# Performance work log

Hardware: AMD Instinct MI355X
Metric: run time of the kernel (lower is better)

## Reference

```python
import jax, jax.numpy as jnp
import numpy as np

B, S, D_IN, D_OUT = 4, 2048, 1024, 1024


def setup_inputs() -> dict:
    key = jax.random.key(0)
    ks = jax.random.split(key, 6)
    scale = 1.0 / np.sqrt(D_IN)
    return {
        "inputs_for_keys": jax.random.normal(ks[0], (B, S, D_IN), jnp.float32),
        "inputs_for_values": jax.random.normal(ks[1], (B, S, D_IN), jnp.float32),
        "inputs_for_queries": jax.random.normal(ks[2], (B, S, D_IN), jnp.float32),
        "WK": jax.random.uniform(ks[3], (D_IN, D_OUT), jnp.float32, -scale, scale),
        "WQ": jax.random.uniform(ks[4], (D_IN, D_OUT), jnp.float32, -scale, scale),
        "WV": jax.random.uniform(ks[5], (D_IN, D_OUT), jnp.float32, -scale, scale),
    }


def reference(inputs_for_keys, inputs_for_values, inputs_for_queries, WK, WQ, WV):
    # QKV projections: [B,S,Din] @ [Din,Dout] -> [B,S,Dout]
    keys = jnp.einsum("bsd,de->bse", inputs_for_keys, WK)
    values = jnp.einsum("bsd,de->bse", inputs_for_values, WV)
    queries = jnp.einsum("bsd,de->bse", inputs_for_queries, WQ)
    d_k = keys.shape[-1]
    # scaled scores [B,S,S]
    scores = jnp.einsum("bqe,bke->bqk", queries, keys) / jnp.sqrt(jnp.float32(d_k))
    # causal mask: position k > q gets -inf (strictly upper triangular)
    q_idx = jnp.arange(S)[:, None]
    k_idx = jnp.arange(S)[None, :]
    scores = jnp.where(k_idx > q_idx, -jnp.inf, scores)
    att = jax.nn.softmax(scores, axis=-1)
    out = jnp.einsum("bqk,bke->bqe", att, values)  # [B,S,Dout]
    return out
```

## Files before the change

kernel.cpp:

```cpp
#include <hip/hip_runtime.h>
#include <stdint.h>


typedef __attribute__((ext_vector_type(8))) short short8;
typedef __attribute__((ext_vector_type(8))) unsigned short ushort8;
typedef __attribute__((ext_vector_type(4))) float f32x4;

__device__ __forceinline__ unsigned short f2bf(float f) {
  union { float f; unsigned u; } v; v.f = f;
  unsigned u = v.u + 0x7FFFu + ((v.u >> 16) & 1u);
  return (unsigned short)(u >> 16);
}
__device__ __forceinline__ float bf2f(unsigned short h) {
  union { unsigned u; float f; } v; v.u = ((unsigned)h) << 16;
  return v.f;
}

__device__ __forceinline__ void gload16(const void* g, void* l) {
  __builtin_amdgcn_global_load_lds(
      (const __attribute__((address_space(1))) unsigned int*)g,
      (__attribute__((address_space(3))) unsigned int*)l, 16, 0, 0);
}

template<int N> __device__ __forceinline__ void vmwait() {
  static_assert(N >= 0 && N <= 8, "vmcnt range");
  if constexpr (N == 0) asm volatile("s_waitcnt vmcnt(0)" ::: "memory");
  else if constexpr (N == 1) asm volatile("s_waitcnt vmcnt(1)" ::: "memory");
  else if constexpr (N == 2) asm volatile("s_waitcnt vmcnt(2)" ::: "memory");
  else if constexpr (N == 3) asm volatile("s_waitcnt vmcnt(3)" ::: "memory");
  else if constexpr (N == 4) asm volatile("s_waitcnt vmcnt(4)" ::: "memory");
  else if constexpr (N == 5) asm volatile("s_waitcnt vmcnt(5)" ::: "memory");
  else if constexpr (N == 6) asm volatile("s_waitcnt vmcnt(6)" ::: "memory");
  else if constexpr (N == 7) asm volatile("s_waitcnt vmcnt(7)" ::: "memory");
  else asm volatile("s_waitcnt vmcnt(8)" ::: "memory");
}
__device__ __forceinline__ void barrier_() { asm volatile("s_barrier" ::: "memory"); }
__device__ __forceinline__ void lgkm0() { asm volatile("s_waitcnt lgkmcnt(0)" ::: "memory"); }

__global__ __launch_bounds__(256)
void cvt3_bf16(const float* __restrict__ Xq, const float* __restrict__ Xk,
               const float* __restrict__ Xv,
               unsigned short* __restrict__ Oq, unsigned short* __restrict__ Ok,
               unsigned short* __restrict__ Ov) {
  const int bx = blockIdx.x;
  const int op = bx >> 12, r = bx & 4095;
  const float* in = op == 0 ? Xq : op == 1 ? Xk : Xv;
  unsigned short* out = op == 0 ? Oq : op == 1 ? Ok : Ov;
  const long i = ((long)r * 256 + threadIdx.x) * 8;
  float4 a = *(const float4*)(in + i);
  float4 b = *(const float4*)(in + i + 4);
  ushort8 rr;
  rr[0] = f2bf(a.x); rr[1] = f2bf(a.y); rr[2] = f2bf(a.z); rr[3] = f2bf(a.w);
  rr[4] = f2bf(b.x); rr[5] = f2bf(b.y); rr[6] = f2bf(b.z); rr[7] = f2bf(b.w);
  *(ushort8*)(out + i) = rr;
}

__global__ __launch_bounds__(256)
void wtrans3(const float* __restrict__ WQ, const float* __restrict__ WK,
             const float* __restrict__ WV,
             unsigned short* __restrict__ WQT, unsigned short* __restrict__ WKT,
             unsigned short* __restrict__ WVT) {
  const int z = blockIdx.z;
  const float* W = z == 0 ? WQ : z == 1 ? WK : WV;
  unsigned short* WT = z == 0 ? WQT : z == 1 ? WKT : WVT;
  const float scale = z == 0 ? 0.03125f : 1.0f;
  __shared__ float t[32][33];
  const int bk = blockIdx.x * 32, be = blockIdx.y * 32;
  const int tx = threadIdx.x, ty = threadIdx.y;
#pragma unroll
  for (int j = 0; j < 32; j += 8)
    t[ty + j][tx] = W[(long)(bk + ty + j) * 1024 + (be + tx)];
  __syncthreads();
#pragma unroll
  for (int j = 0; j < 32; j += 8)
    WT[(long)(be + ty + j) * 1024 + (bk + tx)] = f2bf(t[tx][ty + j] * scale);
}

template<typename CT, int MF, int NF>
__device__ __forceinline__ void gemm_body(const unsigned short* __restrict__ A,
                                          const unsigned short* __restrict__ B,
                                          CT* __restrict__ C,
                                          int bm, int bn, int kmax,
                                          int lda, int ldb, int ldc,
                                          char* AL, char* BL) {
  constexpr int BM = MF * 32, BN = NF * 64;
  constexpr int LA = BM / 128, LB = BN / 128;
  constexpr int V = 2 * LA + LB;

  const int tid = threadIdx.x;
  const int lane = tid & 63, wid = tid >> 6;
  const int wr = wid >> 2, wc = wid & 3;
  const int fr = lane & 15, fq = lane >> 4;
  const int srow = tid >> 2;
  const int scol = (((tid & 3) ^ ((tid >> 3) & 3)) << 3);
  const int m0 = bm * BM, n0 = bn * BN;
  const int nt = kmax >> 6;

  f32x4 acc[MF][NF] = {};

  const unsigned short* As = A + (long)(m0 + srow) * lda + scol;
  const unsigned short* Bs = B + (long)(n0 + srow) * ldb + scol;

  auto stageA = [&](int b, int h, int kt) {
#pragma unroll
    for (int l = 0; l < LA; ++l)
      gload16(As + (long)l * 128 * lda + kt * 64 + h * 32,
              AL + b * (BM * 128) + h * (BM * 64) + l * 8192 + tid * 16);
  };
  auto stageB = [&](int b, int h, int kt) {
#pragma unroll
    for (int l = 0; l < LB; ++l)
      gload16(Bs + (long)l * 128 * ldb + kt * 64 + h * 32,
              BL + b * (BN * 128) + h * (BN * 64) + l * 8192 + tid * 16);
  };

  const int aoff = (wr * (BM / 2) + fr) * 64 + ((fq ^ ((fr >> 1) & 3)) << 4);
  const int boff = (wc * (BN / 4) + fr) * 64 + ((fq ^ ((fr >> 1) & 3)) << 4);
  auto ardf = [&](int b, int kk, int m) -> short8 {
    return *(const short8*)(AL + b * (BM * 128) + kk * (BM * 64) + aoff + m * 1024);
  };
  auto brdf = [&](int b, int kk, int n) -> short8 {
    return *(const short8*)(BL + b * (BN * 128) + kk * (BN * 64) + boff + n * 1024);
  };

  stageA(0, 0, 0); stageB(0, 0, 0); stageA(0, 1, 0); stageB(0, 1, 0);

  for (int u = 0; u < nt; ++u) {
    const int cb = u & 1, nb = cb ^ 1;
    const bool pf = (u + 1 < nt);
    lgkm0();
    barrier_();
    if (pf) { stageA(nb, 0, u + 1); vmwait<V>(); }
    else    { vmwait<LA + LB>(); }
    barrier_();
    short8 bfr[NF], af[MF / 2];
#pragma unroll
    for (int n = 0; n < NF; ++n) bfr[n] = brdf(cb, 0, n);
#pragma unroll
    for (int m = 0; m < MF / 2; ++m) af[m] = ardf(cb, 0, m);
    if (pf) stageB(nb, 0, u + 1);
    __builtin_amdgcn_s_setprio(1);
#pragma unroll
    for (int m = 0; m < MF / 2; ++m)
#pragma unroll
      for (int n = 0; n < NF; ++n)
        acc[m][n] = __builtin_amdgcn_mfma_f32_16x16x32_bf16(af[m], bfr[n], acc[m][n], 0, 0, 0);
    __builtin_amdgcn_s_setprio(0);
#pragma unroll
    for (int m = 0; m < MF / 2; ++m) af[m] = ardf(cb, 0, MF / 2 + m);
    if (pf) stageA(nb, 1, u + 1);
    __builtin_amdgcn_s_setprio(1);
#pragma unroll
    for (int m = 0; m < MF / 2; ++m)
#pragma unroll
      for (int n = 0; n < NF; ++n)
        acc[MF / 2 + m][n] =
            __builtin_amdgcn_mfma_f32_16x16x32_bf16(af[m], bfr[n], acc[MF / 2 + m][n], 0, 0, 0);
    __builtin_amdgcn_s_setprio(0);
    if (pf) vmwait<V>(); else vmwait<0>();
    barrier_();
#pragma unroll
    for (int n = 0; n < NF; ++n) bfr[n] = brdf(cb, 1, n);
#pragma unroll
    for (int m = 0; m < MF / 2; ++m) af[m] = ardf(cb, 1, m);
    if (pf) stageB(nb, 1, u + 1);
    __builtin_amdgcn_s_setprio(1);
#pragma unroll
    for (int m = 0; m < MF / 2; ++m)
#pragma unroll
      for (int n = 0; n < NF; ++n)
        acc[m][n] = __builtin_amdgcn_mfma_f32_16x16x32_bf16(af[m], bfr[n], acc[m][n], 0, 0, 0);
    __builtin_amdgcn_s_setprio(0);
#pragma unroll
    for (int m = 0; m < MF / 2; ++m) af[m] = ardf(cb, 1, MF / 2 + m);
    __builtin_amdgcn_s_setprio(1);
#pragma unroll
    for (int m = 0; m < MF / 2; ++m)
#pragma unroll
      for (int n = 0; n < NF; ++n)
        acc[MF / 2 + m][n] =
            __builtin_amdgcn_mfma_f32_16x16x32_bf16(af[m], bfr[n], acc[MF / 2 + m][n], 0, 0, 0);
    __builtin_amdgcn_s_setprio(0);
  }

#pragma unroll
  for (int m = 0; m < MF; ++m) {
    const int row = m0 + wr * (BM / 2) + m * 16 + fq * 4;
#pragma unroll
    for (int n = 0; n < NF; ++n) {
      const int col = n0 + wc * (BN / 4) + n * 16 + fr;
#pragma unroll
      for (int r = 0; r < 4; ++r) {
        float v = acc[m][n][r];
        if constexpr (sizeof(CT) == 2)
          C[(long)(row + r) * ldc + col] = (CT)f2bf(v);
        else
          C[(long)(row + r) * ldc + col] = (CT)v;
      }
    }
  }
}

__global__ __launch_bounds__(512, 2)
void qkvt_gemm(const unsigned short* __restrict__ Xq, const unsigned short* __restrict__ WQT,
               unsigned short* __restrict__ Q,
               const unsigned short* __restrict__ Xk, const unsigned short* __restrict__ WKT,
               unsigned short* __restrict__ Kk,
               const unsigned short* __restrict__ WVT, const unsigned short* __restrict__ Xv,
               unsigned short* __restrict__ VT) {
  __shared__ __align__(16) char pool[131072];
  const int id = (blockIdx.x & 7) * 32 + (blockIdx.x >> 3);
  if (id < 128)
    gemm_body<unsigned short, 8, 4>(Xq, WQT, Q, id >> 2, id & 3, 1024,
                                    1024, 1024, 1024, pool, pool + 65536);
  else
    gemm_body<unsigned short, 8, 4>(Xk, WKT, Kk, (id - 128) >> 2, id & 3, 1024,
                                    1024, 1024, 1024, pool, pool + 65536);
  __syncthreads();
  gemm_body<unsigned short, 4, 4>(WVT, Xv, VT, id >> 5, id & 31, 1024,
                                  1024, 1024, 8192, pool, pool + 32768);
}

__global__ __launch_bounds__(512, 2)
void scores_gemm(const unsigned short* __restrict__ Q, const unsigned short* __restrict__ K,
                 unsigned short* __restrict__ S) {
  __shared__ __align__(16) char pool[131072];
  const int id = (blockIdx.x & 7) * 32 + (blockIdx.x >> 3);
  const int bz = id >> 6, r = id & 63, bm = r >> 3, bn = r & 7;
  if (bn > bm) return;
  gemm_body<unsigned short, 8, 4>(Q + (long)bz * 2048 * 1024, K + (long)bz * 2048 * 1024,
                                  S + (long)bz * 2048 * 2048, bm, bn, 1024,
                                  1024, 1024, 2048, pool, pool + 65536);
}

__global__ __launch_bounds__(512, 4)
void pv_gemm(const unsigned short* __restrict__ P, const unsigned short* __restrict__ VT,
             float* __restrict__ O) {
  __shared__ __align__(16) char pool[65536];
  const int b = blockIdx.x;
  int bm, r;
  if (b < 256) { bm = 15 - (b >> 5); r = b & 31; }
  else         { bm = (b - 256) >> 5; r = b & 31; }
  const int bn = r & 7, bz = r >> 3;
  gemm_body<float, 4, 2>(P + (long)bz * 2048 * 2048, VT + (long)bz * 2048,
                         O + (long)bz * 2048 * 1024, bm, bn, (bm + 1) * 128,
                         2048, 8192, 1024, pool, pool + 32768);
}

__global__ __launch_bounds__(256)
void softmax_causal(unsigned short* __restrict__ P) {
  const int row = blockIdx.x;
  const int q = row & 2047;
  unsigned short* p = P + (long)row * 2048;
  const int nfill = ((q >> 7) + 1) << 7;
  const int tid = threadIdx.x;
  const int lane = tid & 63, wid = tid >> 6;
  const int i0 = tid * 8;
  __shared__ float red[8];

  float v[8];
  float lmax = -3.0e38f;
  if (i0 <= q) {
    ushort8 v8 = *(const ushort8*)(p + i0);
#pragma unroll
    for (int j = 0; j < 8; ++j) {
      float f = bf2f(v8[j]);
      f = (i0 + j <= q) ? f : -3.0e38f;
      v[j] = f;
      lmax = fmaxf(lmax, f);
    }
  } else {
#pragma unroll
    for (int j = 0; j < 8; ++j) v[j] = -3.0e38f;
  }
#pragma unroll
  for (int off = 1; off < 64; off <<= 1)
    lmax = fmaxf(lmax, __shfl_xor(lmax, off));
  if (lane == 0) red[wid] = lmax;
  __syncthreads();
  const float mx = fmaxf(fmaxf(red[0], red[1]), fmaxf(red[2], red[3]));

  float lsum = 0.f;
#pragma unroll
  for (int j = 0; j < 8; ++j) {
    float e = __expf(v[j] - mx);
    v[j] = e;
    lsum += e;
  }
#pragma unroll
  for (int off = 1; off < 64; off <<= 1)
    lsum += __shfl_xor(lsum, off);
  if (lane == 0) red[4 + wid] = lsum;
  __syncthreads();
  const float inv = 1.0f / (red[4] + red[5] + red[6] + red[7]);

  if (i0 < nfill) {
    ushort8 r;
#pragma unroll
    for (int j = 0; j < 8; ++j)
      r[j] = (i0 + j <= q) ? f2bf(v[j] * inv) : (unsigned short)0;
    *(ushort8*)(p + i0) = r;
  }
}

extern "C" void kernel_launch(void* const* d_in, const int* in_sizes, int n_in,
                              void* d_out, int out_size, void* d_ws, size_t ws_size,
                              hipStream_t stream) {
  const float* Xk = (const float*)d_in[0];
  const float* Xv = (const float*)d_in[1];
  const float* Xq = (const float*)d_in[2];
  const float* WK = (const float*)d_in[3];
  const float* WQ = (const float*)d_in[4];
  const float* WV = (const float*)d_in[5];
  float* out = (float*)d_out;

  unsigned short* ws = (unsigned short*)d_ws;
  const long NE = 8L * 1024 * 1024;
  unsigned short* Xqb = ws + 0 * NE;
  unsigned short* Xkb = ws + 1 * NE;
  unsigned short* Xvb = ws + 2 * NE;
  unsigned short* Qb  = ws + 3 * NE;
  unsigned short* Kb  = ws + 4 * NE;
  unsigned short* VTb = ws + 5 * NE;
  unsigned short* WQT = ws + 6 * NE;
  unsigned short* WKT = WQT + 1024 * 1024;
  unsigned short* WVT = WKT + 1024 * 1024;
  unsigned short* Sc  = ws;

  dim3 b256(256), b512(512);
  cvt3_bf16<<<12288, b256, 0, stream>>>(Xq, Xk, Xv, Xqb, Xkb, Xvb);
  wtrans3<<<dim3(32, 32, 3), dim3(32, 8), 0, stream>>>(WQ, WK, WV, WQT, WKT, WVT);
  qkvt_gemm<<<256, b512, 0, stream>>>(Xqb, WQT, Qb, Xkb, WKT, Kb, WVT, Xvb, VTb);
  scores_gemm<<<256, b512, 0, stream>>>(Qb, Kb, Sc);
  softmax_causal<<<8192, b256, 0, stream>>>(Sc);
  pv_gemm<<<512, b512, 0, stream>>>(Sc, VTb, out);
}
```

Baseline: 157.2 us.

## Restructure GEMM main loop to whole-tile prefetch and shrink scores tiles

```diff
diff --git a/kernel.cpp b/kernel.cpp
--- a/kernel.cpp
+++ b/kernel.cpp
@@ -23,7 +23,7 @@
 }
 
 template<int N> __device__ __forceinline__ void vmwait() {
-  static_assert(N >= 0 && N <= 8, "vmcnt range");
+  static_assert(N >= 0 && N <= 16, "vmcnt range");
   if constexpr (N == 0) asm volatile("s_waitcnt vmcnt(0)" ::: "memory");
   else if constexpr (N == 1) asm volatile("s_waitcnt vmcnt(1)" ::: "memory");
   else if constexpr (N == 2) asm volatile("s_waitcnt vmcnt(2)" ::: "memory");
@@ -32,7 +32,10 @@
   else if constexpr (N == 5) asm volatile("s_waitcnt vmcnt(5)" ::: "memory");
   else if constexpr (N == 6) asm volatile("s_waitcnt vmcnt(6)" ::: "memory");
   else if constexpr (N == 7) asm volatile("s_waitcnt vmcnt(7)" ::: "memory");
-  else asm volatile("s_waitcnt vmcnt(8)" ::: "memory");
+  else if constexpr (N == 8) asm volatile("s_waitcnt vmcnt(8)" ::: "memory");
+  else if constexpr (N == 10) asm volatile("s_waitcnt vmcnt(10)" ::: "memory");
+  else if constexpr (N == 12) asm volatile("s_waitcnt vmcnt(12)" ::: "memory");
+  else asm volatile("s_waitcnt vmcnt(16)" ::: "memory");
 }
 __device__ __forceinline__ void barrier_() { asm volatile("s_barrier" ::: "memory"); }
 __device__ __forceinline__ void lgkm0() { asm volatile("s_waitcnt lgkmcnt(0)" ::: "memory"); }
@@ -85,7 +88,9 @@
                                           char* AL, char* BL) {
   constexpr int BM = MF * 32, BN = NF * 64;
   constexpr int LA = BM / 128, LB = BN / 128;
-  constexpr int V = 2 * LA + LB;
+  constexpr int SA = 2 * (LA + LB);
+  constexpr int NH = (NF >= 4) ? 2 : 1;
+  constexpr int NS = NF / NH;
 
   const int tid = threadIdx.x;
   const int lane = tid & 63, wid = tid >> 6;
@@ -101,17 +106,18 @@
   const unsigned short* As = A + (long)(m0 + srow) * lda + scol;
   const unsigned short* Bs = B + (long)(n0 + srow) * ldb + scol;
 
-  auto stageA = [&](int b, int h, int kt) {
-#pragma unroll
-    for (int l = 0; l < LA; ++l)
-      gload16(As + (long)l * 128 * lda + kt * 64 + h * 32,
-              AL + b * (BM * 128) + h * (BM * 64) + l * 8192 + tid * 16);
-  };
-  auto stageB = [&](int b, int h, int kt) {
-#pragma unroll
-    for (int l = 0; l < LB; ++l)
-      gload16(Bs + (long)l * 128 * ldb + kt * 64 + h * 32,
-              BL + b * (BN * 128) + h * (BN * 64) + l * 8192 + tid * 16);
+  auto stageTile = [&](int b, int kt) {
+#pragma unroll
+    for (int h = 0; h < 2; ++h) {
+#pragma unroll
+      for (int l = 0; l < LA; ++l)
+        gload16(As + (long)l * 128 * lda + kt * 64 + h * 32,
+                AL + b * (BM * 128) + h * (BM * 64) + l * 8192 + tid * 16);
+#pragma unroll
+      for (int l = 0; l < LB; ++l)
+        gload16(Bs + (long)l * 128 * ldb + kt * 64 + h * 32,
+                BL + b * (BN * 128) + h * (BN * 64) + l * 8192 + tid * 16);
+    }
   };
 
   const int aoff = (wr * (BM / 2) + fr) * 64 + ((fq ^ ((fr >> 1) & 3)) << 4);
@@ -123,64 +129,44 @@
     return *(const short8*)(BL + b * (BN * 128) + kk * (BN * 64) + boff + n * 1024);
   };
 
-  stageA(0, 0, 0); stageB(0, 0, 0); stageA(0, 1, 0); stageB(0, 1, 0);
+  stageTile(0, 0);
 
   for (int u = 0; u < nt; ++u) {
     const int cb = u & 1, nb = cb ^ 1;
-    const bool pf = (u + 1 < nt);
     lgkm0();
     barrier_();
-    if (pf) { stageA(nb, 0, u + 1); vmwait<V>(); }
-    else    { vmwait<LA + LB>(); }
+    if (u + 1 < nt) { stageTile(nb, u + 1); vmwait<SA>(); }
+    else            { vmwait<0>(); }
     barrier_();
-    short8 bfr[NF], af[MF / 2];
-#pragma unroll
-    for (int n = 0; n < NF; ++n) bfr[n] = brdf(cb, 0, n);
-#pragma unroll
-    for (int m = 0; m < MF / 2; ++m) af[m] = ardf(cb, 0, m);
-    if (pf) stageB(nb, 0, u + 1);
-    __builtin_amdgcn_s_setprio(1);
-#pragma unroll
-    for (int m = 0; m < MF / 2; ++m)
-#pragma unroll
-      for (int n = 0; n < NF; ++n)
-        acc[m][n] = __builtin_amdgcn_mfma_f32_16x16x32_bf16(af[m], bfr[n], acc[m][n], 0, 0, 0);
-    __builtin_amdgcn_s_setprio(0);
-#pragma unroll
-    for (int m = 0; m < MF / 2; ++m) af[m] = ardf(cb, 0, MF / 2 + m);
-    if (pf) stageA(nb, 1, u + 1);
-    __builtin_amdgcn_s_setprio(1);
-#pragma unroll
-    for (int m = 0; m < MF / 2; ++m)
-#pragma unroll
-      for (int n = 0; n < NF; ++n)
-        acc[MF / 2 + m][n] =
-            __builtin_amdgcn_mfma_f32_16x16x32_bf16(af[m], bfr[n], acc[MF / 2 + m][n], 0, 0, 0);
-    __builtin_amdgcn_s_setprio(0);
-    if (pf) vmwait<V>(); else vmwait<0>();
-    barrier_();
-#pragma unroll
-    for (int n = 0; n < NF; ++n) bfr[n] = brdf(cb, 1, n);
-#pragma unroll
-    for (int m = 0; m < MF / 2; ++m) af[m] = ardf(cb, 1, m);
-    if (pf) stageB(nb, 1, u + 1);
-    __builtin_amdgcn_s_setprio(1);
-#pragma unroll
-    for (int m = 0; m < MF / 2; ++m)
-#pragma unroll
-      for (int n = 0; n < NF; ++n)
-        acc[m][n] = __builtin_amdgcn_mfma_f32_16x16x32_bf16(af[m], bfr[n], acc[m][n], 0, 0, 0);
-    __builtin_amdgcn_s_setprio(0);
-#pragma unroll
-    for (int m = 0; m < MF / 2; ++m) af[m] = ardf(cb, 1, MF / 2 + m);
-    __builtin_amdgcn_s_setprio(1);
-#pragma unroll
-    for (int m = 0; m < MF / 2; ++m)
-#pragma unroll
-      for (int n = 0; n < NF; ++n)
-        acc[MF / 2 + m][n] =
-            __builtin_amdgcn_mfma_f32_16x16x32_bf16(af[m], bfr[n], acc[MF / 2 + m][n], 0, 0, 0);
-    __builtin_amdgcn_s_setprio(0);
+#pragma unroll
+    for (int mh = 0; mh < 2; ++mh) {
+#pragma unroll
+      for (int nh = 0; nh < NH; ++nh) {
+        short8 a0[MF / 2], a1[MF / 2], b0[NS], b1[NS];
+#pragma unroll
+        for (int m = 0; m < MF / 2; ++m) {
+          a0[m] = ardf(cb, 0, mh * (MF / 2) + m);
+          a1[m] = ardf(cb, 1, mh * (MF / 2) + m);
+        }
+#pragma unroll
+        for (int n = 0; n < NS; ++n) {
+          b0[n] = brdf(cb, 0, nh * NS + n);
+          b1[n] = brdf(cb, 1, nh * NS + n);
+        }
+        __builtin_amdgcn_s_setprio(1);
+#pragma unroll
+        for (int m = 0; m < MF / 2; ++m) {
+#pragma unroll
+          for (int n = 0; n < NS; ++n) {
+            const int M = mh * (MF / 2) + m, N = nh * NS + n;
+            acc[M][N] = __builtin_amdgcn_mfma_f32_16x16x32_bf16(a0[m], b0[n], acc[M][N], 0, 0, 0);
+            acc[M][N] = __builtin_amdgcn_mfma_f32_16x16x32_bf16(a1[m], b1[n], acc[M][N], 0, 0, 0);
+          }
+        }
+        __builtin_amdgcn_s_setprio(0);
+        if (!(mh == 1 && nh == NH - 1)) barrier_();
+      }
+    }
   }
 
 #pragma unroll
@@ -221,16 +207,19 @@
                                   1024, 1024, 8192, pool, pool + 32768);
 }
 
-__global__ __launch_bounds__(512, 2)
+__global__ __launch_bounds__(512, 4)
 void scores_gemm(const unsigned short* __restrict__ Q, const unsigned short* __restrict__ K,
                  unsigned short* __restrict__ S) {
-  __shared__ __align__(16) char pool[131072];
-  const int id = (blockIdx.x & 7) * 32 + (blockIdx.x >> 3);
-  const int bz = id >> 6, r = id & 63, bm = r >> 3, bn = r & 7;
-  if (bn > bm) return;
-  gemm_body<unsigned short, 8, 4>(Q + (long)bz * 2048 * 1024, K + (long)bz * 2048 * 1024,
+  __shared__ __align__(16) char pool[65536];
+  const int gid = (blockIdx.x & 7) * 68 + (blockIdx.x >> 3);
+  const int bz = gid / 136, t = gid - bz * 136;
+  int bm = (int)((__fsqrt_rn(8.0f * t + 1.0f) - 1.0f) * 0.5f);
+  while ((bm + 1) * (bm + 2) / 2 <= t) ++bm;
+  while (bm * (bm + 1) / 2 > t) --bm;
+  const int bn = t - bm * (bm + 1) / 2;
+  gemm_body<unsigned short, 4, 2>(Q + (long)bz * 2048 * 1024, K + (long)bz * 2048 * 1024,
                                   S + (long)bz * 2048 * 2048, bm, bn, 1024,
-                                  1024, 1024, 2048, pool, pool + 65536);
+                                  1024, 1024, 2048, pool, pool + 32768);
 }
 
 __global__ __launch_bounds__(512, 4)
@@ -331,7 +320,7 @@
   cvt3_bf16<<<12288, b256, 0, stream>>>(Xq, Xk, Xv, Xqb, Xkb, Xvb);
   wtrans3<<<dim3(32, 32, 3), dim3(32, 8), 0, stream>>>(WQ, WK, WV, WQT, WKT, WVT);
   qkvt_gemm<<<256, b512, 0, stream>>>(Xqb, WQT, Qb, Xkb, WKT, Kb, WVT, Xvb, VTb);
-  scores_gemm<<<256, b512, 0, stream>>>(Qb, Kb, Sc);
+  scores_gemm<<<544, b512, 0, stream>>>(Qb, Kb, Sc);
   softmax_causal<<<8192, b256, 0, stream>>>(Sc);
   pv_gemm<<<512, b512, 0, stream>>>(Sc, VTb, out);
 }
```

Measured after the change: 173.0 us. +10.0%, slower.

## Switch GEMMs to 32x32x16 MFMA and retile causal scores grid

Applied to the files above, without the earlier changes.

```diff
diff --git a/kernel.cpp b/kernel.cpp
--- a/kernel.cpp
+++ b/kernel.cpp
@@ -4,7 +4,7 @@
 
 typedef __attribute__((ext_vector_type(8))) short short8;
 typedef __attribute__((ext_vector_type(8))) unsigned short ushort8;
-typedef __attribute__((ext_vector_type(4))) float f32x4;
+typedef __attribute__((ext_vector_type(16))) float f32x16;
 
 __device__ __forceinline__ unsigned short f2bf(float f) {
   union { float f; unsigned u; } v; v.f = f;
@@ -86,17 +86,21 @@
   constexpr int BM = MF * 32, BN = NF * 64;
   constexpr int LA = BM / 128, LB = BN / 128;
   constexpr int V = 2 * LA + LB;
+  constexpr int MFR = MF / 2;
+  constexpr int NFR = NF / 2;
+  constexpr int MH = (MFR >= 2) ? MFR / 2 : 1;
 
   const int tid = threadIdx.x;
   const int lane = tid & 63, wid = tid >> 6;
   const int wr = wid >> 2, wc = wid & 3;
-  const int fr = lane & 15, fq = lane >> 4;
+  const int fr = lane & 31;
+  const int fq = lane >> 5;
   const int srow = tid >> 2;
   const int scol = (((tid & 3) ^ ((tid >> 3) & 3)) << 3);
   const int m0 = bm * BM, n0 = bn * BN;
   const int nt = kmax >> 6;
 
-  f32x4 acc[MF][NF] = {};
+  f32x16 acc[MFR][NFR] = {};
 
   const unsigned short* As = A + (long)(m0 + srow) * lda + scol;
   const unsigned short* Bs = B + (long)(n0 + srow) * ldb + scol;
@@ -114,13 +118,15 @@
               BL + b * (BN * 128) + h * (BN * 64) + l * 8192 + tid * 16);
   };
 
-  const int aoff = (wr * (BM / 2) + fr) * 64 + ((fq ^ ((fr >> 1) & 3)) << 4);
-  const int boff = (wc * (BN / 4) + fr) * 64 + ((fq ^ ((fr >> 1) & 3)) << 4);
-  auto ardf = [&](int b, int kk, int m) -> short8 {
-    return *(const short8*)(AL + b * (BM * 128) + kk * (BM * 64) + aoff + m * 1024);
+  auto ard = [&](int b, int kk, int m, int ks) -> short8 {
+    const int row = wr * (BM / 2) + m * 32 + fr;
+    const int slot = (ks * 2 + fq) ^ ((fr >> 1) & 3);
+    return *(const short8*)(AL + b * (BM * 128) + kk * (BM * 64) + row * 64 + (slot << 4));
   };
-  auto brdf = [&](int b, int kk, int n) -> short8 {
-    return *(const short8*)(BL + b * (BN * 128) + kk * (BN * 64) + boff + n * 1024);
+  auto brd = [&](int b, int kk, int n, int ks) -> short8 {
+    const int row = wc * (BN / 4) + n * 32 + fr;
+    const int slot = (ks * 2 + fq) ^ ((fr >> 1) & 3);
+    return *(const short8*)(BL + b * (BN * 128) + kk * (BN * 64) + row * 64 + (slot << 4));
   };
 
   stageA(0, 0, 0); stageB(0, 0, 0); stageA(0, 1, 0); stageB(0, 1, 0);
@@ -133,69 +139,76 @@
     if (pf) { stageA(nb, 0, u + 1); vmwait<V>(); }
     else    { vmwait<LA + LB>(); }
     barrier_();
-    short8 bfr[NF], af[MF / 2];
-#pragma unroll
-    for (int n = 0; n < NF; ++n) bfr[n] = brdf(cb, 0, n);
-#pragma unroll
-    for (int m = 0; m < MF / 2; ++m) af[m] = ardf(cb, 0, m);
+    short8 bfr[NFR][2], af[MH][2];
+#pragma unroll
+    for (int n = 0; n < NFR; ++n) { bfr[n][0] = brd(cb, 0, n, 0); bfr[n][1] = brd(cb, 0, n, 1); }
+#pragma unroll
+    for (int m = 0; m < MH; ++m) { af[m][0] = ard(cb, 0, m, 0); af[m][1] = ard(cb, 0, m, 1); }
     if (pf) stageB(nb, 0, u + 1);
     __builtin_amdgcn_s_setprio(1);
 #pragma unroll
-    for (int m = 0; m < MF / 2; ++m)
-#pragma unroll
-      for (int n = 0; n < NF; ++n)
-        acc[m][n] = __builtin_amdgcn_mfma_f32_16x16x32_bf16(af[m], bfr[n], acc[m][n], 0, 0, 0);
+    for (int m = 0; m < MH; ++m)
+#pragma unroll
+      for (int n = 0; n < NFR; ++n) {
+        acc[m][n] = __builtin_amdgcn_mfma_f32_32x32x16_bf16(af[m][0], bfr[n][0], acc[m][n], 0, 0, 0);
+        acc[m][n] = __builtin_amdgcn_mfma_f32_32x32x16_bf16(af[m][1], bfr[n][1], acc[m][n], 0, 0, 0);
+      }
     __builtin_amdgcn_s_setprio(0);
 #pragma unroll
-    for (int m = 0; m < MF / 2; ++m) af[m] = ardf(cb, 0, MF / 2 + m);
+    for (int m = 0; m < MFR - MH; ++m) { af[m][0] = ard(cb, 0, MH + m, 0); af[m][1] = ard(cb, 0, MH + m, 1); }
     if (pf) stageA(nb, 1, u + 1);
     __builtin_amdgcn_s_setprio(1);
 #pragma unroll
-    for (int m = 0; m < MF / 2; ++m)
-#pragma unroll
-      for (int n = 0; n < NF; ++n)
-        acc[MF / 2 + m][n] =
-            __builtin_amdgcn_mfma_f32_16x16x32_bf16(af[m], bfr[n], acc[MF / 2 + m][n], 0, 0, 0);
+    for (int m = 0; m < MFR - MH; ++m)
+#pragma unroll
+      for (int n = 0; n < NFR; ++n) {
+        acc[MH + m][n] = __builtin_amdgcn_mfma_f32_32x32x16_bf16(af[m][0], bfr[n][0], acc[MH + m][n], 0, 0, 0);
+        acc[MH + m][n] = __builtin_amdgcn_mfma_f32_32x32x16_bf16(af[m][1], bfr[n][1], acc[MH + m][n], 0, 0, 0);
+      }
     __builtin_amdgcn_s_setprio(0);
     if (pf) vmwait<V>(); else vmwait<0>();
     barrier_();
 #pragma unroll
-    for (int n = 0; n < NF; ++n) bfr[n] = brdf(cb, 1, n);
-#pragma unroll
-    for (int m = 0; m < MF / 2; ++m) af[m] = ardf(cb, 1, m);
+    for (int n = 0; n < NFR; ++n) { bfr[n][0] = brd(cb, 1, n, 0); bfr[n][1] = brd(cb, 1, n, 1); }
+#pragma unroll
+    for (int m = 0; m < MH; ++m) { af[m][0] = ard(cb, 1, m, 0); af[m][1] = ard(cb, 1, m, 1); }
     if (pf) stageB(nb, 1, u + 1);
     __builtin_amdgcn_s_setprio(1);
 #pragma unroll
-    for (int m = 0; m < MF / 2; ++m)
-#pragma unroll
-      for (int n = 0; n < NF; ++n)
-        acc[m][n] = __builtin_amdgcn_mfma_f32_16x16x32_bf16(af[m], bfr[n], acc[m][n], 0, 0, 0);
+    for (int m = 0; m < MH; ++m)
+#pragma unroll
+      for (int n = 0; n < NFR; ++n) {
+        acc[m][n] = __builtin_amdgcn_mfma_f32_32x32x16_bf16(af[m][0], bfr[n][0], acc[m][n], 0, 0, 0);
+        acc[m][n] = __builtin_amdgcn_mfma_f32_32x32x16_bf16(af[m][1], bfr[n][1], acc[m][n], 0, 0, 0);
+      }
     __builtin_amdgcn_s_setprio(0);
 #pragma unroll
-    for (int m = 0; m < MF / 2; ++m) af[m] = ardf(cb, 1, MF / 2 + m);
+    for (int m = 0; m < MFR - MH; ++m) { af[m][0] = ard(cb, 1, MH + m, 0); af[m][1] = ard(cb, 1, MH + m, 1); }
     __builtin_amdgcn_s_setprio(1);
 #pragma unroll
-    for (int m = 0; m < MF / 2; ++m)
-#pragma unroll
-      for (int n = 0; n < NF; ++n)
-        acc[MF / 2 + m][n] =
-            __builtin_amdgcn_mfma_f32_16x16x32_bf16(af[m], bfr[n], acc[MF / 2 + m][n], 0, 0, 0);
+    for (int m = 0; m < MFR - MH; ++m)
+#pragma unroll
+      for (int n = 0; n < NFR; ++n) {
+        acc[MH + m][n] = __builtin_amdgcn_mfma_f32_32x32x16_bf16(af[m][0], bfr[n][0], acc[MH + m][n], 0, 0, 0);
+        acc[MH + m][n] = __builtin_amdgcn_mfma_f32_32x32x16_bf16(af[m][1], bfr[n][1], acc[MH + m][n], 0, 0, 0);
+      }
     __builtin_amdgcn_s_setprio(0);
   }
 
 #pragma unroll
-  for (int m = 0; m < MF; ++m) {
-    const int row = m0 + wr * (BM / 2) + m * 16 + fq * 4;
-#pragma unroll
-    for (int n = 0; n < NF; ++n) {
-      const int col = n0 + wc * (BN / 4) + n * 16 + fr;
-#pragma unroll
-      for (int r = 0; r < 4; ++r) {
+  for (int m = 0; m < MFR; ++m) {
+    const int row0 = m0 + wr * (BM / 2) + m * 32 + fq * 4;
+#pragma unroll
+    for (int n = 0; n < NFR; ++n) {
+      const int col = n0 + wc * (BN / 4) + n * 32 + fr;
+#pragma unroll
+      for (int r = 0; r < 16; ++r) {
+        const int row = row0 + (r & 3) + 8 * (r >> 2);
         float v = acc[m][n][r];
         if constexpr (sizeof(CT) == 2)
-          C[(long)(row + r) * ldc + col] = (CT)f2bf(v);
+          C[(long)row * ldc + col] = (CT)f2bf(v);
         else
-          C[(long)(row + r) * ldc + col] = (CT)v;
+          C[(long)row * ldc + col] = (CT)v;
       }
     }
   }
@@ -221,16 +234,19 @@
                                   1024, 1024, 8192, pool, pool + 32768);
 }
 
-__global__ __launch_bounds__(512, 2)
+__global__ __launch_bounds__(512, 4)
 void scores_gemm(const unsigned short* __restrict__ Q, const unsigned short* __restrict__ K,
                  unsigned short* __restrict__ S) {
-  __shared__ __align__(16) char pool[131072];
-  const int id = (blockIdx.x & 7) * 32 + (blockIdx.x >> 3);
-  const int bz = id >> 6, r = id & 63, bm = r >> 3, bn = r & 7;
-  if (bn > bm) return;
-  gemm_body<unsigned short, 8, 4>(Q + (long)bz * 2048 * 1024, K + (long)bz * 2048 * 1024,
+  __shared__ __align__(16) char pool[65536];
+  const int gid = (blockIdx.x & 7) * 68 + (blockIdx.x >> 3);
+  const int bz = gid / 136, t = gid - bz * 136;
+  int bm = (int)((__fsqrt_rn(8.0f * t + 1.0f) - 1.0f) * 0.5f);
+  while ((bm + 1) * (bm + 2) / 2 <= t) ++bm;
+  while (bm * (bm + 1) / 2 > t) --bm;
+  const int bn = t - bm * (bm + 1) / 2;
+  gemm_body<unsigned short, 4, 2>(Q + (long)bz * 2048 * 1024, K + (long)bz * 2048 * 1024,
                                   S + (long)bz * 2048 * 2048, bm, bn, 1024,
-                                  1024, 1024, 2048, pool, pool + 65536);
+                                  1024, 1024, 2048, pool, pool + 32768);
 }
 
 __global__ __launch_bounds__(512, 4)
@@ -331,7 +347,7 @@
   cvt3_bf16<<<12288, b256, 0, stream>>>(Xq, Xk, Xv, Xqb, Xkb, Xvb);
   wtrans3<<<dim3(32, 32, 3), dim3(32, 8), 0, stream>>>(WQ, WK, WV, WQT, WKT, WVT);
   qkvt_gemm<<<256, b512, 0, stream>>>(Xqb, WQT, Qb, Xkb, WKT, Kb, WVT, Xvb, VTb);
-  scores_gemm<<<256, b512, 0, stream>>>(Qb, Kb, Sc);
+  scores_gemm<<<544, b512, 0, stream>>>(Qb, Kb, Sc);
   softmax_causal<<<8192, b256, 0, stream>>>(Sc);
   pv_gemm<<<512, b512, 0, stream>>>(Sc, VTb, out);
 }
```

Result: no change. 160.1 us (+1.8%).

## Fuse fp32-to-bf16 input conversion into QKV GEMM and retile causal scores GEMM

Applied to the files above, without the earlier changes.

```diff
diff --git a/kernel.cpp b/kernel.cpp
--- a/kernel.cpp
+++ b/kernel.cpp
@@ -5,6 +5,7 @@
 typedef __attribute__((ext_vector_type(8))) short short8;
 typedef __attribute__((ext_vector_type(8))) unsigned short ushort8;
 typedef __attribute__((ext_vector_type(4))) float f32x4;
+typedef __attribute__((ext_vector_type(4))) unsigned int uint4v;
 
 __device__ __forceinline__ unsigned short f2bf(float f) {
   union { float f; unsigned u; } v; v.f = f;
@@ -14,6 +15,9 @@
 __device__ __forceinline__ float bf2f(unsigned short h) {
   union { unsigned u; float f; } v; v.u = ((unsigned)h) << 16;
   return v.f;
+}
+__device__ __forceinline__ unsigned pk2(float lo, float hi) {
+  return (unsigned)f2bf(lo) | ((unsigned)f2bf(hi) << 16);
 }
 
 __device__ __forceinline__ void gload16(const void* g, void* l) {
@@ -36,24 +40,6 @@
 }
 __device__ __forceinline__ void barrier_() { asm volatile("s_barrier" ::: "memory"); }
 __device__ __forceinline__ void lgkm0() { asm volatile("s_waitcnt lgkmcnt(0)" ::: "memory"); }
-
-__global__ __launch_bounds__(256)
-void cvt3_bf16(const float* __restrict__ Xq, const float* __restrict__ Xk,
-               const float* __restrict__ Xv,
-               unsigned short* __restrict__ Oq, unsigned short* __restrict__ Ok,
-               unsigned short* __restrict__ Ov) {
-  const int bx = blockIdx.x;
-  const int op = bx >> 12, r = bx & 4095;
-  const float* in = op == 0 ? Xq : op == 1 ? Xk : Xv;
-  unsigned short* out = op == 0 ? Oq : op == 1 ? Ok : Ov;
-  const long i = ((long)r * 256 + threadIdx.x) * 8;
-  float4 a = *(const float4*)(in + i);
-  float4 b = *(const float4*)(in + i + 4);
-  ushort8 rr;
-  rr[0] = f2bf(a.x); rr[1] = f2bf(a.y); rr[2] = f2bf(a.z); rr[3] = f2bf(a.w);
-  rr[4] = f2bf(b.x); rr[5] = f2bf(b.y); rr[6] = f2bf(b.z); rr[7] = f2bf(b.w);
-  *(ushort8*)(out + i) = rr;
-}
 
 __global__ __launch_bounds__(256)
 void wtrans3(const float* __restrict__ WQ, const float* __restrict__ WK,
@@ -201,36 +187,178 @@
   }
 }
 
+template<int MF, int NF, bool BREG>
+__device__ __forceinline__ void gemm_fused(const float* __restrict__ X,
+                                           const unsigned short* __restrict__ Wt,
+                                           unsigned short* __restrict__ C,
+                                           int bm, int bn, int kmax,
+                                           int ldx, int ldw, int ldc,
+                                           char* AL, char* BL) {
+  constexpr int BM = MF * 32, BN = NF * 64;
+  constexpr int DROWS = BREG ? BM : BN;
+  constexpr int RROWS = BREG ? BN : BM;
+  constexpr int DR = DROWS / 128;
+  constexpr int D = 2 * DR;
+  constexpr int WW = RROWS / 128;
+  constexpr int R = 4 * WW;
+  static_assert(WW == 2, "reg operand must be 256 rows");
+
+  const int tid = threadIdx.x;
+  const int lane = tid & 63, wid = tid >> 6;
+  const int wr = wid >> 2, wc = wid & 3;
+  const int fr = lane & 15, fq = lane >> 4;
+  const int srow = tid >> 2;
+  const int key = (tid >> 3) & 3;
+  const int scol = ((tid & 3) ^ key) << 3;
+  const int m0 = bm * BM, n0 = bn * BN;
+  const int nt = kmax >> 6;
+
+  f32x4 acc[MF][NF] = {};
+
+  char* DL = BREG ? AL : BL;
+  char* RL = BREG ? BL : AL;
+  const int d0 = BREG ? m0 : n0;
+  const int r0 = BREG ? n0 : m0;
+  const unsigned short* Ws = Wt + (long)(d0 + srow) * ldw + scol;
+  const float* Xs = X + (long)(r0 + srow) * ldx + scol;
+
+  auto stageDMA = [&](int b, int kt) {
+#pragma unroll
+    for (int h = 0; h < 2; ++h)
+#pragma unroll
+      for (int l = 0; l < DR; ++l)
+        gload16(Ws + (long)l * 128 * ldw + kt * 64 + h * 32,
+                DL + b * (DROWS * 128) + h * (DROWS * 64) + l * 8192 + tid * 16);
+  };
+
+  float4 rv[2][2][2];
+  auto issueREG = [&](int kt) {
+#pragma unroll
+    for (int h = 0; h < 2; ++h)
+#pragma unroll
+      for (int w = 0; w < 2; ++w) {
+        const float* p = Xs + (long)w * 128 * ldx + kt * 64 + h * 32;
+        rv[h][w][0] = *(const float4*)p;
+        rv[h][w][1] = *(const float4*)(p + 4);
+      }
+  };
+  auto writeREG = [&](int b) {
+#pragma unroll
+    for (int h = 0; h < 2; ++h)
+#pragma unroll
+      for (int w = 0; w < 2; ++w) {
+        uint4v q;
+        q[0] = pk2(rv[h][w][0].x, rv[h][w][0].y);
+        q[1] = pk2(rv[h][w][0].z, rv[h][w][0].w);
+        q[2] = pk2(rv[h][w][1].x, rv[h][w][1].y);
+        q[3] = pk2(rv[h][w][1].z, rv[h][w][1].w);
+        *(uint4v*)(RL + b * (RROWS * 128) + h * (RROWS * 64) + w * 8192 + tid * 16) = q;
+      }
+  };
+
+  const int aoff = (wr * (BM / 2) + fr) * 64 + ((fq ^ ((fr >> 1) & 3)) << 4);
+  const int boff = (wc * (BN / 4) + fr) * 64 + ((fq ^ ((fr >> 1) & 3)) << 4);
+  auto ardf = [&](int b, int kk, int m) -> short8 {
+    return *(const short8*)(AL + b * (BM * 128) + kk * (BM * 64) + aoff + m * 1024);
+  };
+  auto brdf = [&](int b, int kk, int n) -> short8 {
+    return *(const short8*)(BL + b * (BN * 128) + kk * (BN * 64) + boff + n * 1024);
+  };
+
+  auto compute = [&](int cb) {
+    short8 bfr[NF], af[MF / 2];
+#pragma unroll
+    for (int kk = 0; kk < 2; ++kk) {
+#pragma unroll
+      for (int n = 0; n < NF; ++n) bfr[n] = brdf(cb, kk, n);
+#pragma unroll
+      for (int m = 0; m < MF / 2; ++m) af[m] = ardf(cb, kk, m);
+      __builtin_amdgcn_s_setprio(1);
+#pragma unroll
+      for (int m = 0; m < MF / 2; ++m)
+#pragma unroll
+        for (int n = 0; n < NF; ++n)
+          acc[m][n] = __builtin_amdgcn_mfma_f32_16x16x32_bf16(af[m], bfr[n], acc[m][n], 0, 0, 0);
+      __builtin_amdgcn_s_setprio(0);
+#pragma unroll
+      for (int m = 0; m < MF / 2; ++m) af[m] = ardf(cb, kk, MF / 2 + m);
+      __builtin_amdgcn_s_setprio(1);
+#pragma unroll
+      for (int m = 0; m < MF / 2; ++m)
+#pragma unroll
+        for (int n = 0; n < NF; ++n)
+          acc[MF / 2 + m][n] =
+              __builtin_amdgcn_mfma_f32_16x16x32_bf16(af[m], bfr[n], acc[MF / 2 + m][n], 0, 0, 0);
+      __builtin_amdgcn_s_setprio(0);
+    }
+  };
+
+  issueREG(0);
+  stageDMA(0, 0);
+  vmwait<D>();
+  writeREG(0);
+  if (nt > 1) issueREG(1);
+  if (nt > 1) vmwait<R>(); else vmwait<0>();
+  lgkm0(); barrier_();
+
+  for (int u = 0; u < nt; ++u) {
+    const int cb = u & 1, nb = cb ^ 1;
+    if (u + 1 < nt) { stageDMA(nb, u + 1); vmwait<D>(); }
+    else            { vmwait<0>(); }
+    if (u + 1 < nt) writeREG(nb);
+    if (u + 2 < nt) issueREG(u + 2);
+    compute(cb);
+    if (u + 2 < nt)      vmwait<R>();
+    else                 vmwait<0>();
+    lgkm0(); barrier_();
+  }
+
+#pragma unroll
+  for (int m = 0; m < MF; ++m) {
+    const int row = m0 + wr * (BM / 2) + m * 16 + fq * 4;
+#pragma unroll
+    for (int n = 0; n < NF; ++n) {
+      const int col = n0 + wc * (BN / 4) + n * 16 + fr;
+#pragma unroll
+      for (int r = 0; r < 4; ++r)
+        C[(long)(row + r) * ldc + col] = f2bf(acc[m][n][r]);
+    }
+  }
+}
+
 __global__ __launch_bounds__(512, 2)
-void qkvt_gemm(const unsigned short* __restrict__ Xq, const unsigned short* __restrict__ WQT,
+void qkvt_gemm(const float* __restrict__ Xq, const unsigned short* __restrict__ WQT,
                unsigned short* __restrict__ Q,
-               const unsigned short* __restrict__ Xk, const unsigned short* __restrict__ WKT,
+               const float* __restrict__ Xk, const unsigned short* __restrict__ WKT,
                unsigned short* __restrict__ Kk,
-               const unsigned short* __restrict__ WVT, const unsigned short* __restrict__ Xv,
+               const unsigned short* __restrict__ WVT, const float* __restrict__ Xv,
                unsigned short* __restrict__ VT) {
   __shared__ __align__(16) char pool[131072];
   const int id = (blockIdx.x & 7) * 32 + (blockIdx.x >> 3);
-  if (id < 128)
-    gemm_body<unsigned short, 8, 4>(Xq, WQT, Q, id >> 2, id & 3, 1024,
-                                    1024, 1024, 1024, pool, pool + 65536);
-  else
-    gemm_body<unsigned short, 8, 4>(Xk, WKT, Kk, (id - 128) >> 2, id & 3, 1024,
-                                    1024, 1024, 1024, pool, pool + 65536);
+  const float* X = (id < 128) ? Xq : Xk;
+  const unsigned short* W = (id < 128) ? WQT : WKT;
+  unsigned short* Cc = (id < 128) ? Q : Kk;
+  const int r = id & 127;
+  gemm_fused<8, 4, false>(X, W, Cc, r >> 2, r & 3, 1024,
+                          1024, 1024, 1024, pool, pool + 65536);
   __syncthreads();
-  gemm_body<unsigned short, 4, 4>(WVT, Xv, VT, id >> 5, id & 31, 1024,
-                                  1024, 1024, 8192, pool, pool + 32768);
-}
-
-__global__ __launch_bounds__(512, 2)
+  gemm_fused<4, 4, true>(Xv, WVT, VT, id >> 5, id & 31, 1024,
+                         1024, 1024, 8192, pool, pool + 32768);
+}
+
+__global__ __launch_bounds__(512, 4)
 void scores_gemm(const unsigned short* __restrict__ Q, const unsigned short* __restrict__ K,
                  unsigned short* __restrict__ S) {
-  __shared__ __align__(16) char pool[131072];
-  const int id = (blockIdx.x & 7) * 32 + (blockIdx.x >> 3);
-  const int bz = id >> 6, r = id & 63, bm = r >> 3, bn = r & 7;
-  if (bn > bm) return;
-  gemm_body<unsigned short, 8, 4>(Q + (long)bz * 2048 * 1024, K + (long)bz * 2048 * 1024,
+  __shared__ __align__(16) char pool[65536];
+  const int gid = (blockIdx.x & 7) * 68 + (blockIdx.x >> 3);
+  const int bz = gid / 136, t = gid - bz * 136;
+  int bm = (int)((__fsqrt_rn(8.0f * t + 1.0f) - 1.0f) * 0.5f);
+  while ((bm + 1) * (bm + 2) / 2 <= t) ++bm;
+  while (bm * (bm + 1) / 2 > t) --bm;
+  const int bn = t - bm * (bm + 1) / 2;
+  gemm_body<unsigned short, 4, 2>(Q + (long)bz * 2048 * 1024, K + (long)bz * 2048 * 1024,
                                   S + (long)bz * 2048 * 2048, bm, bn, 1024,
-                                  1024, 1024, 2048, pool, pool + 65536);
+                                  1024, 1024, 2048, pool, pool + 32768);
 }
 
 __global__ __launch_bounds__(512, 4)
@@ -316,22 +444,18 @@
 
   unsigned short* ws = (unsigned short*)d_ws;
   const long NE = 8L * 1024 * 1024;
-  unsigned short* Xqb = ws + 0 * NE;
-  unsigned short* Xkb = ws + 1 * NE;
-  unsigned short* Xvb = ws + 2 * NE;
-  unsigned short* Qb  = ws + 3 * NE;
-  unsigned short* Kb  = ws + 4 * NE;
-  unsigned short* VTb = ws + 5 * NE;
-  unsigned short* WQT = ws + 6 * NE;
+  unsigned short* Sc  = ws;
+  unsigned short* Qb  = ws + 2 * NE;
+  unsigned short* Kb  = ws + 3 * NE;
+  unsigned short* VTb = ws + 4 * NE;
+  unsigned short* WQT = ws + 5 * NE;
   unsigned short* WKT = WQT + 1024 * 1024;
   unsigned short* WVT = WKT + 1024 * 1024;
-  unsigned short* Sc  = ws;
 
   dim3 b256(256), b512(512);
-  cvt3_bf16<<<12288, b256, 0, stream>>>(Xq, Xk, Xv, Xqb, Xkb, Xvb);
   wtrans3<<<dim3(32, 32, 3), dim3(32, 8), 0, stream>>>(WQ, WK, WV, WQT, WKT, WVT);
-  qkvt_gemm<<<256, b512, 0, stream>>>(Xqb, WQT, Qb, Xkb, WKT, Kb, WVT, Xvb, VTb);
-  scores_gemm<<<256, b512, 0, stream>>>(Qb, Kb, Sc);
+  qkvt_gemm<<<256, b512, 0, stream>>>(Xq, WQT, Qb, Xk, WKT, Kb, WVT, Xv, VTb);
+  scores_gemm<<<544, b512, 0, stream>>>(Qb, Kb, Sc);
   softmax_causal<<<8192, b256, 0, stream>>>(Sc);
   pv_gemm<<<512, b512, 0, stream>>>(Sc, VTb, out);
 }
```

Result: slower. 166.0 us (+5.6%).
